# Kernel tuning notes

Hardware: AMD Instinct MI355X
Metric: run time of the kernel (lower is better)

The kernel has to match this reference:

```python
import jax, jax.numpy as jnp
import numpy as np

K = 3           # kernel_size
N_LAYERS = 2    # n_layers; circuit applies StronglyEntanglingLayers(weights) N_LAYERS times
STRIDE = 2
N_QUBITS = K * K  # 9 qubits -> 512-dim statevector


def _apply_1q(state, U, q):
    """Apply 2x2 unitary U (shared (2,2) or per-batch (P,2,2)) to qubit q.
    state: (P,) + (2,)*N_QUBITS complex64."""
    s = jnp.moveaxis(state, 1 + q, -1)
    if U.ndim == 3:
        s = jnp.einsum('pji,p...i->p...j', U, s)
    else:
        s = jnp.einsum('ji,...i->...j', U, s)
    return jnp.moveaxis(s, -1, 1 + q)


def _apply_cnot(state, c, t):
    """CNOT with control c, target t on state (P,)+(2,)*n."""
    s0 = jnp.take(state, 0, axis=1 + c)
    s1 = jnp.take(state, 1, axis=1 + c)
    t_ax = 1 + t if t < c else t  # target axis after control axis removed
    s1 = jnp.flip(s1, axis=t_ax)
    return jnp.stack([s0, s1], axis=1 + c)


def _rot_matrix(phi, theta, omega):
    """PennyLane Rot(phi, theta, omega) = RZ(omega) RY(theta) RZ(phi)."""
    c = jnp.cos(theta / 2)
    s = jnp.sin(theta / 2)
    u00 = jnp.exp(-0.5j * (phi + omega)) * c
    u01 = -jnp.exp(0.5j * (phi - omega)) * s
    u10 = jnp.exp(-0.5j * (phi - omega)) * s
    u11 = jnp.exp(0.5j * (phi + omega)) * c
    return jnp.stack([jnp.stack([u00, u01]), jnp.stack([u10, u11])]).astype(jnp.complex64)


def _circuit(angles, weights):
    """angles: (P, N_QUBITS) float32. Returns PauliZ expvals (P, N_QUBITS) float32."""
    P = angles.shape[0]
    n = N_QUBITS
    state = jnp.zeros((P, 2 ** n), jnp.complex64).at[:, 0].set(1.0)
    state = state.reshape((P,) + (2,) * n)
    # AngleEmbedding (default rotation = RX) per wire, angle varies per patch
    half = angles / 2
    cos = jnp.cos(half)
    sin = jnp.sin(half)
    for q in range(n):
        c = cos[:, q].astype(jnp.complex64)
        s = (-1j * sin[:, q]).astype(jnp.complex64)
        U = jnp.stack([jnp.stack([c, s], -1), jnp.stack([s, c], -1)], -2)  # (P,2,2)
        state = _apply_1q(state, U, q)
    # Faithful to source: StronglyEntanglingLayers(weights) applied N_LAYERS times,
    # each containing N_LAYERS internal layers (Rot on each wire + CNOT ring).
    for _ in range(N_LAYERS):
        for l in range(N_LAYERS):
            for q in range(n):
                state = _apply_1q(
                    state,
                    _rot_matrix(weights[l, q, 0], weights[l, q, 1], weights[l, q, 2]),
                    q,
                )
            r = (l % (n - 1)) + 1  # PennyLane default ranges
            for q in range(n):
                state = _apply_cnot(state, q, (q + r) % n)
    probs = state.real ** 2 + state.imag ** 2  # (P,)+(2,)*n
    exps = []
    for q in range(n):
        axes = tuple(ax for ax in range(1, n + 1) if ax != 1 + q)
        m = probs.sum(axis=axes)  # (P, 2)
        exps.append(m[:, 0] - m[:, 1])
    return jnp.stack(exps, axis=1)


def _forward(input, weights):
    B, _, H, W = input.shape
    out = (H - K) // STRIDE + 1
    starts = jnp.arange(out) * STRIDE
    win = starts[:, None] + jnp.arange(K)  # (out, K) row/col start offsets
    x = input[:, 0]  # (B, H, W), channels asserted == 1
    # vectorized sliding-window patch extraction: (B, out, out, K, K)
    patches = x[:, win[:, None, :, None], win[None, :, None, :]]
    angles = patches.reshape(B * out * out, N_QUBITS)  # row-major flatten, matches torch.flatten
    ev = _circuit(angles, weights)  # (B*out*out, N_QUBITS)
    ev = ev.reshape(B, out * out, N_QUBITS).transpose(0, 2, 1)
    return ev.reshape(B, N_QUBITS, out, out).astype(jnp.float32)


def setup_inputs() -> dict:
    key = jax.random.key(0)
    k1, k2 = jax.random.split(key)
    inp = jax.random.normal(k1, (8, 1, 128, 128), dtype=jnp.float32)
    weights = jax.random.uniform(k2, (N_LAYERS, N_QUBITS, 3), dtype=jnp.float32,
                                 minval=0.0, maxval=2 * np.pi)
    return {"input": inp, "weights": weights}


def reference(input, weights):
    return _forward(input, weights)
```

## Files before the change

kernel.cpp:

```cpp
#include <hip/hip_runtime.h>


namespace {

constexpr int OUT_HW = 63;
constexpr int PPB = 2;
constexpr int N_PATCH_TOTAL = 8 * OUT_HW * OUT_HW;

typedef _Float16 h2 __attribute__((ext_vector_type(2)));
typedef __fp16  hw2 __attribute__((ext_vector_type(2)));

__device__ __forceinline__ int h2i(h2 v) { return __builtin_bit_cast(int, v); }
__device__ __forceinline__ h2  i2h(int v) { return __builtin_bit_cast(h2, v); }
__device__ __forceinline__ h2  swap_h2(h2 v) { return __builtin_shufflevector(v, v, 1, 0); }

__device__ __forceinline__ int bperm_i(int addr, int v) {
    return __builtin_amdgcn_ds_bpermute(addr, v);
}

template<int M>
__device__ __forceinline__ int shfl_i(int v, int lane) {
    if constexpr (M < 32)
        return __builtin_amdgcn_ds_swizzle(v, 0x1F | (M << 10));
    else
        return bperm_i((lane << 2) ^ 128, v);
}
template<int M>
__device__ __forceinline__ float shfl_f(float v, int lane) {
    return __int_as_float(shfl_i<M>(__float_as_int(v), lane));
}

template<int C, int T>
__device__ __forceinline__ void cnot_h(h2 (&a)[8])
{
    constexpr int cm = 1 << C, tm = 1 << T;
    #pragma unroll
    for (int r = 0; r < 8; ++r) {
        if ((r & cm) && !(r & tm)) {
            const int r1 = r | tm;
            const h2 t = a[r]; a[r] = a[r1]; a[r1] = t;
        }
    }
}

__device__ __forceinline__ void ring1_partial_h(h2 (&a)[8], int lane)
{
    cnot_h<0,1>(a);
    cnot_h<1,2>(a);
    const int sA = (lane ^ ((lane & 31) << 1)) << 2;
    const int sB = sA ^ 4;
    #pragma unroll
    for (int r = 0; r < 8; ++r)
        a[r] = i2h(bperm_i((r & 4) ? sB : sA, h2i(a[r])));
}

__device__ __forceinline__ void ring2_partial_h(h2 (&a)[8], int lane)
{
    cnot_h<0,2>(a);
    const int s0 = (lane ^ ((lane & 15) << 2)) << 2;
    #pragma unroll
    for (int r = 0; r < 8; ++r) {
        const int ad = s0 ^ (((r >> 1) & 1) << 2) ^ (((r >> 2) & 1) << 3);
        a[r] = i2h(bperm_i(ad, h2i(a[r])));
    }
}

__device__ __forceinline__ void apply_diag_h(h2 (&a)[8],
                                             const int* __restrict__ dtab,
                                             int dbase, int lane)
{
    #pragma unroll
    for (int r = 0; r < 8; ++r) {
        const int idx = (dbase + r * 64 + lane) * 2;
        const h2 cc = i2h(dtab[idx]);
        const h2 ns = i2h(dtab[idx + 1]);
        a[r] = cc * a[r] + ns * swap_h2(a[r]);
    }
}

__device__ __forceinline__ void load_diag(h2 (&cc)[8], h2 (&ns)[8],
                                          const int* __restrict__ dtab,
                                          int dbase, int lane)
{
    #pragma unroll
    for (int r = 0; r < 8; ++r) {
        const int idx = (dbase + r * 64 + lane) * 2;
        cc[r] = i2h(dtab[idx]);
        ns[r] = i2h(dtab[idx + 1]);
    }
}

__device__ __forceinline__ void apply_diag_pre(h2 (&a)[8],
                                               const h2 (&cc)[8],
                                               const h2 (&ns)[8])
{
    #pragma unroll
    for (int r = 0; r < 8; ++r)
        a[r] = cc[r] * a[r] + ns[r] * swap_h2(a[r]);
}

template<int QM>
__device__ __forceinline__ void regY_h(h2 (&a)[8], h2 A2, h2 B2, h2 C2, h2 D2)
{
    #pragma unroll
    for (int r = 0; r < 8; ++r) {
        if (!(r & QM)) {
            const int r1 = r | QM;
            const h2 x0 = a[r], x1 = a[r1];
            a[r]  = A2 * x0 + B2 * x1;
            a[r1] = C2 * x0 + D2 * x1;
        }
    }
}

template<int LM>
__device__ __forceinline__ void laneY_h(h2 (&a)[8], int lane, h2 c2, h2 sp2)
{
    #pragma unroll
    for (int r = 0; r < 8; ++r) {
        const h2 p = i2h(shfl_i<LM>(h2i(a[r]), lane));
        a[r] = c2 * a[r] + sp2 * p;
    }
}

__device__ __forceinline__ void apply_Y_h(h2 (&a)[8], int lane,
                                          const int* __restrict__ yt,
                                          bool sw0, bool sw1)
{
    {   const int cc = yt[0], ss = yt[1], ns = yt[2];
        regY_h<1>(a, i2h(sw0 ? ns : cc), i2h(sw0 ? cc : ns),
                     i2h(sw0 ? cc : ss), i2h(sw0 ? ss : cc)); }
    {   const int cc = yt[3], ss = yt[4], ns = yt[5];
        regY_h<2>(a, i2h(sw1 ? ns : cc), i2h(sw1 ? cc : ns),
                     i2h(sw1 ? cc : ss), i2h(sw1 ? ss : cc)); }
    {   regY_h<4>(a, i2h(yt[6]), i2h(yt[8]), i2h(yt[7]), i2h(yt[6])); }
    {   laneY_h<1>(a, lane, i2h(yt[9]),  i2h((lane & 1)        ? yt[10] : yt[11])); }
    {   laneY_h<2>(a, lane, i2h(yt[12]), i2h(((lane >> 1) & 1) ? yt[13] : yt[14])); }
    {   laneY_h<4>(a, lane, i2h(yt[15]), i2h(((lane >> 2) & 1) ? yt[16] : yt[17])); }
    {   laneY_h<8>(a, lane, i2h(yt[18]), i2h(((lane >> 3) & 1) ? yt[19] : yt[20])); }
    {   laneY_h<16>(a, lane, i2h(yt[21]), i2h(((lane >> 4) & 1) ? yt[22] : yt[23])); }
    {   laneY_h<32>(a, lane, i2h(yt[24]), i2h(((lane >> 5) & 1) ? yt[25] : yt[26])); }
}

__global__ void precomp_kernel(const float* __restrict__ w, float* __restrict__ ws)
{
    const int tid = threadIdx.x;
    float* rot = ws;
    int* ytab = (int*)(ws + 144);
    int* dtab = (int*)(ws + 208);
    if (tid < 18) {
        const float phi = w[tid*3 + 0], theta = w[tid*3 + 1], omega = w[tid*3 + 2];
        const float ct = cosf(0.5f * theta), st = sinf(0.5f * theta);
        const float apo = 0.5f * (phi + omega), amo = 0.5f * (phi - omega);
        const float ca = cosf(apo), sa = sinf(apo);
        const float cm = cosf(amo), sm = sinf(amo);
        float* m = rot + tid * 8;
        m[0] =  ca * ct; m[1] = -sa * ct;
        m[2] = -cm * st; m[3] = -sm * st;
        m[4] =  cm * st; m[5] = -sm * st;
        m[6] =  ca * ct; m[7] =  sa * ct;
        h2 cc; cc.x = (_Float16)ct;  cc.y = (_Float16)ct;
        h2 ss; ss.x = (_Float16)st;  ss.y = (_Float16)st;
        h2 ns; ns.x = (_Float16)(-st); ns.y = (_Float16)(-st);
        ytab[tid*3 + 0] = h2i(cc);
        ytab[tid*3 + 1] = h2i(ss);
        ytab[tid*3 + 2] = h2i(ns);
    }
    if (tid < 192) {
        const int vmask[9] = {0x1FE,0x003,0x007,0x00F,0x01F,0x03F,0x07F,0x0FF,0x1FF};
        const int wmask[9] = {0x0AB,0x157,0x005,0x00A,0x015,0x02A,0x055,0x0AA,0x155};
        const int d = tid >> 6, lane = tid & 63;
        for (int r = 0; r < 8; ++r) {
            const int p = (lane << 3) | r;
            float ang = 0.f;
            for (int q = 0; q < 9; ++q) {
                if (d == 0) {
                    const float lam = -0.5f * w[(9 + q)*3 + 0];
                    ang += (__popc(p & vmask[q]) & 1) ? -lam : lam;
                } else if (d == 1) {
                    const float lam = -0.5f * w[q*3 + 0];
                    ang += (__popc(p & wmask[q]) & 1) ? -lam : lam;
                    const float lm2 = -0.5f * w[(9 + q)*3 + 2];
                    ang += ((p >> q) & 1) ? -lm2 : lm2;
                } else {
                    const float lam = -0.5f * w[(9 + q)*3 + 0];
                    ang += (__popc(p & vmask[q]) & 1) ? -lam : lam;
                    const float lm2 = -0.5f * w[q*3 + 2];
                    ang += ((p >> q) & 1) ? -lm2 : lm2;
                }
            }
            const float c = cosf(ang), s = sinf(ang);
            h2 cc;  cc.x = (_Float16)c;    cc.y = (_Float16)c;
            h2 nsp; nsp.x = (_Float16)(-s); nsp.y = (_Float16)s;
            const int idx = ((d*8 + r)*64 + lane)*2;
            dtab[idx + 0] = h2i(cc);
            dtab[idx + 1] = h2i(nsp);
        }
    }
}

__global__ __launch_bounds__(PPB * 64, 8) void qconv_kernel(
    const float* __restrict__ x,
    const float* __restrict__ ws,
    float* __restrict__ out)
{
    const float* rot  = ws;
    const int* ytab = (const int*)(ws + 144);
    const int* dtab = (const int*)(ws + 208);

    const int lane  = threadIdx.x & 63;
    const int wv    = threadIdx.x >> 6;
    const int patch = blockIdx.x * PPB + wv;

    const int b   = patch / (OUT_HW * OUT_HW);
    const int rem = patch - b * (OUT_HW * OUT_HW);
    const int oy  = rem / OUT_HW;
    const int ox  = rem - oy * OUT_HW;

    __shared__ __align__(16) float abtab[PPB][36];
    if (lane < 36) {
        const int q = lane >> 2, comp = lane & 3;
        const float ang = x[b * 16384 + (oy * 2 + q / 3) * 128 + (ox * 2 + q % 3)];
        float s, c;
        __sincosf(0.5f * ang, &s, &c);
        const float* R = rot + 8 * q;
        float v;
        if      (comp == 0) v = c*R[0] + s*R[3];
        else if (comp == 1) v = c*R[1] - s*R[2];
        else if (comp == 2) v = c*R[4] + s*R[7];
        else                v = c*R[5] - s*R[6];
        abtab[wv][lane] = v;
    }
    __builtin_amdgcn_wave_barrier();

    float ab[36];
    {
        const float4* src = reinterpret_cast<const float4*>(&abtab[wv][0]);
        float4* dst = reinterpret_cast<float4*>(ab);
        #pragma unroll
        for (int j = 0; j < 9; ++j) dst[j] = src[j];
    }

    float ar[8], ai[8];
    {
        float Lr = 1.0f, Li = 0.0f;
        #pragma unroll
        for (int q = 3; q < 9; ++q) {
            const int bit = (lane >> (q - 3)) & 1;
            const float fr = bit ? ab[4*q + 2] : ab[4*q + 0];
            const float fi = bit ? ab[4*q + 3] : ab[4*q + 1];
            const float nr = Lr*fr - Li*fi;
            const float ni = Lr*fi + Li*fr;
            Lr = nr; Li = ni;
        }
        float c01r[4], c01i[4];
        #pragma unroll
        for (int j = 0; j < 4; ++j) {
            const float f0r = (j & 1) ? ab[2] : ab[0];
            const float f0i = (j & 1) ? ab[3] : ab[1];
            const float f1r = (j & 2) ? ab[6] : ab[4];
            const float f1i = (j & 2) ? ab[7] : ab[5];
            c01r[j] = f0r*f1r - f0i*f1i;
            c01i[j] = f0r*f1i + f0i*f1r;
        }
        float hr[4], hi[4];
        #pragma unroll
        for (int j = 0; j < 4; ++j) {
            hr[j] = c01r[j]*Lr - c01i[j]*Li;
            hi[j] = c01r[j]*Li + c01i[j]*Lr;
        }
        #pragma unroll
        for (int r = 0; r < 8; ++r) {
            const float f2r = (r & 4) ? ab[10] : ab[8];
            const float f2i = (r & 4) ? ab[11] : ab[9];
            ar[r] = hr[r & 3]*f2r - hi[r & 3]*f2i;
            ai[r] = hr[r & 3]*f2i + hi[r & 3]*f2r;
        }
    }

    h2 a[8];
    #pragma unroll
    for (int r = 0; r < 8; ++r)
        a[r] = __builtin_bit_cast(h2, __builtin_amdgcn_cvt_pkrtz(ar[r], ai[r]));

    const bool b4 = ((lane >> 4) & 1) != 0;
    const bool b5 = ((lane >> 5) & 1) != 0;

    h2 dcc[8], dns[8];
    apply_diag_h(a, dtab, 0 * 512, lane);
    load_diag(dcc, dns, dtab, 1 * 512, lane);
    ring1_partial_h(a, lane);
    apply_Y_h(a, lane, ytab + 27, b5, false);
    apply_diag_pre(a, dcc, dns);
    load_diag(dcc, dns, dtab, 2 * 512, lane);
    ring2_partial_h(a, lane);
    apply_Y_h(a, lane, ytab + 0, b4, b5);
    apply_diag_pre(a, dcc, dns);
    ring1_partial_h(a, lane);
    apply_Y_h(a, lane, ytab + 27, b5, false);

    float p[8];
    #pragma unroll
    for (int r = 0; r < 8; ++r) {
#if __has_builtin(__builtin_amdgcn_fdot2)
        p[r] = __builtin_amdgcn_fdot2(__builtin_bit_cast(hw2, a[r]),
                                      __builtin_bit_cast(hw2, a[r]), 0.0f, false);
#else
        const float xr = (float)a[r].x, xi = (float)a[r].y;
        p[r] = xr*xr + xi*xi;
#endif
    }

    const float t03 = p[0]+p[3], t12 = p[1]+p[2], t47 = p[4]+p[7], t56 = p[5]+p[6];
    float S3 = (t03 + t47) - (t12 + t56);
    float S7 = (t03 + t56) - (t12 + t47);
    const float u02 = p[0]+p[2], u13 = p[1]+p[3], u57 = p[5]+p[7], u46 = p[4]+p[6];
    float S5 = (u02 + u57) - (u13 + u46);
    const float v01 = p[0]+p[1], v23 = p[2]+p[3], v45 = p[4]+p[5], v67 = p[6]+p[7];
    float S2 = (v01 + v45) - (v23 + v67);

    const int sm0 = (lane & 1) << 31;
    const int sm1 = ((lane >> 1) & 1) << 31;
    const int sm2 = ((lane >> 2) & 1) << 31;
    const int sm3 = ((lane >> 3) & 1) << 31;
    const int sm4 = ((lane >> 4) & 1) << 31;
    const int sm5 = ((lane >> 5) & 1) << 31;
#define WHT_STAGE(M, SM) { \
    const float q3 = shfl_f<M>(S3, lane), q7 = shfl_f<M>(S7, lane); \
    const float q5 = shfl_f<M>(S5, lane), q2 = shfl_f<M>(S2, lane); \
    S3 = q3 + __int_as_float(__float_as_int(S3) ^ (SM)); \
    S7 = q7 + __int_as_float(__float_as_int(S7) ^ (SM)); \
    S5 = q5 + __int_as_float(__float_as_int(S5) ^ (SM)); \
    S2 = q2 + __int_as_float(__float_as_int(S2) ^ (SM)); }
    WHT_STAGE(1,  sm0)
    WHT_STAGE(2,  sm1)
    WHT_STAGE(4,  sm2)
    WHT_STAGE(8,  sm3)
    WHT_STAGE(16, sm4)
    WHT_STAGE(32, sm5)
#undef WHT_STAGE

    const int base = b * 9;
    const int pix  = oy * OUT_HW + ox;
    int chA = -1; float vA = 0.f;
    if (lane == 0x00) { chA = 2; vA = S5; }
    if (lane == 0x02) { chA = 4; vA = S5; }
    if (lane == 0x0A) { chA = 6; vA = S5; }
    if (lane == 0x2A) { chA = 8; vA = S5; }
    if (lane == 0x01) { chA = 3; vA = S2; }
    if (lane == 0x05) { chA = 5; vA = S2; }
    if (lane == 0x15) { chA = 7; vA = S2; }
    if (chA >= 0)
        out[(base + chA) * (OUT_HW * OUT_HW) + pix] = vA;
    if (lane == 0x15)
        out[(base + 0) * (OUT_HW * OUT_HW) + pix] = S3;
    if (lane == 0x2A)
        out[(base + 1) * (OUT_HW * OUT_HW) + pix] = S7;
}

}

extern "C" void kernel_launch(void* const* d_in, const int* in_sizes, int n_in,
                              void* d_out, int out_size, void* d_ws, size_t ws_size,
                              hipStream_t stream)
{
    const float* x = (const float*)d_in[0];
    const float* w = (const float*)d_in[1];
    float* ws = (float*)d_ws;
    float* out = (float*)d_out;

    precomp_kernel<<<1, 256, 0, stream>>>(w, ws);
    qconv_kernel<<<N_PATCH_TOTAL / PPB, PPB * 64, 0, stream>>>(x, ws, out);
}
```

Measured before the change: 112.2 us.

## Use permlane swaps for lane shuffles, raise patches per block, share setup

Replaces the xor-32 and xor-16 cross-lane shuffles with the permlane32/permlane16 swap builtins when the compiler provides them, in place of the LDS-based bpermute and swizzle paths. Raises patches per block from 2 to 4. Spreads the per-patch angle/rotation table setup across all threads of the block, which needs a block-wide __syncthreads in place of a wave barrier. The aim is cheaper shuffles in the inner gate loop and better setup utilisation, at the cost of a block barrier and a larger block. The xor trick used to pull out the swapped value assumes particular swap semantics.

```diff
diff --git a/kernel.cpp b/kernel.cpp
--- a/kernel.cpp
+++ b/kernel.cpp
@@ -4,11 +4,12 @@
 namespace {
 
 constexpr int OUT_HW = 63;
-constexpr int PPB = 2;
+constexpr int PPB = 4;
 constexpr int N_PATCH_TOTAL = 8 * OUT_HW * OUT_HW;
 
 typedef _Float16 h2 __attribute__((ext_vector_type(2)));
 typedef __fp16  hw2 __attribute__((ext_vector_type(2)));
+typedef unsigned int u2 __attribute__((ext_vector_type(2)));
 
 __device__ __forceinline__ int h2i(h2 v) { return __builtin_bit_cast(int, v); }
 __device__ __forceinline__ h2  i2h(int v) { return __builtin_bit_cast(h2, v); }
@@ -20,10 +21,25 @@
 
 template<int M>
 __device__ __forceinline__ int shfl_i(int v, int lane) {
-    if constexpr (M < 32)
+    if constexpr (M == 32) {
+#if __has_builtin(__builtin_amdgcn_permlane32_swap)
+        const u2 r = __builtin_amdgcn_permlane32_swap((unsigned)v, (unsigned)v,
+                                                      false, false);
+        return v ^ (int)r.x ^ (int)r.y;
+#else
+        return bperm_i((lane << 2) ^ 128, v);
+#endif
+    } else if constexpr (M == 16) {
+#if __has_builtin(__builtin_amdgcn_permlane16_swap)
+        const u2 r = __builtin_amdgcn_permlane16_swap((unsigned)v, (unsigned)v,
+                                                      false, false);
+        return v ^ (int)r.x ^ (int)r.y;
+#else
+        return __builtin_amdgcn_ds_swizzle(v, 0x1F | (16 << 10));
+#endif
+    } else {
         return __builtin_amdgcn_ds_swizzle(v, 0x1F | (M << 10));
-    else
-        return bperm_i((lane << 2) ^ 128, v);
+    }
 }
 template<int M>
 __device__ __forceinline__ float shfl_f(float v, int lane) {
@@ -218,20 +234,29 @@
     const int ox  = rem - oy * OUT_HW;
 
     __shared__ __align__(16) float abtab[PPB][36];
-    if (lane < 36) {
-        const int q = lane >> 2, comp = lane & 3;
-        const float ang = x[b * 16384 + (oy * 2 + q / 3) * 128 + (ox * 2 + q % 3)];
-        float s, c;
-        __sincosf(0.5f * ang, &s, &c);
-        const float* R = rot + 8 * q;
-        float v;
-        if      (comp == 0) v = c*R[0] + s*R[3];
-        else if (comp == 1) v = c*R[1] - s*R[2];
-        else if (comp == 2) v = c*R[4] + s*R[7];
-        else                v = c*R[5] - s*R[6];
-        abtab[wv][lane] = v;
-    }
-    __builtin_amdgcn_wave_barrier();
+    {
+        const int t = threadIdx.x;
+        if (t < PPB * 36) {
+            const int tw = t / 36, j = t - tw * 36;
+            const int q = j >> 2, comp = j & 3;
+            const int tp   = blockIdx.x * PPB + tw;
+            const int tb   = tp / (OUT_HW * OUT_HW);
+            const int trem = tp - tb * (OUT_HW * OUT_HW);
+            const int toy  = trem / OUT_HW;
+            const int tox  = trem - toy * OUT_HW;
+            const float ang = x[tb * 16384 + (toy * 2 + q / 3) * 128 + (tox * 2 + q % 3)];
+            float s, c;
+            __sincosf(0.5f * ang, &s, &c);
+            const float* R = rot + 8 * q;
+            float v;
+            if      (comp == 0) v = c*R[0] + s*R[3];
+            else if (comp == 1) v = c*R[1] - s*R[2];
+            else if (comp == 2) v = c*R[4] + s*R[7];
+            else                v = c*R[5] - s*R[6];
+            abtab[tw][j] = v;
+        }
+    }
+    __syncthreads();
 
     float ab[36];
     {
```

After: 124.4 us. 10.9% more time.
